# Kernel optimization log

Hardware: AMD Instinct MI355X
Metric: run time of the kernel (lower is better)

Reference implementation:

```python
import jax, jax.numpy as jnp
import numpy as np

EMBED_DIM = 512
NUM_HEADS = 8
HEAD_DIM = EMBED_DIM // NUM_HEADS  # 64


def setup_inputs() -> dict:
    key = jax.random.key(0)
    ks = jax.random.split(key, 11)
    B, S, E, dh = 4, 2048, EMBED_DIM, HEAD_DIM
    s_small = 1.0 / np.sqrt(dh)
    s_big = 1.0 / np.sqrt(E)
    return {
        "Q": jax.random.normal(ks[0], (B, S, E), jnp.float32),
        "K": jax.random.normal(ks[1], (B, S, E), jnp.float32),
        "V": jax.random.normal(ks[2], (B, S, E), jnp.float32),
        "Wq_w": jax.random.normal(ks[3], (dh, dh), jnp.float32) * s_small,
        "Wq_b": jnp.zeros((dh,), jnp.float32),
        "Wk_w": jax.random.normal(ks[4], (dh, dh), jnp.float32) * s_small,
        "Wk_b": jnp.zeros((dh,), jnp.float32),
        "Wv_w": jax.random.normal(ks[5], (dh, dh), jnp.float32) * s_small,
        "Wv_b": jnp.zeros((dh,), jnp.float32),
        "Wo_w": jax.random.normal(ks[6], (E, E), jnp.float32) * s_big,
        "Wo_b": jnp.zeros((E,), jnp.float32),
    }


def reference(Q, K, V, Wq_w, Wq_b, Wk_w, Wk_b, Wv_w, Wv_b, Wo_w, Wo_b):
    B, S, E = Q.shape
    H, dh = NUM_HEADS, HEAD_DIM
    # split heads: [B,S,E] -> [B,S,H,dh]; per-head shared linear (torch y = x @ W.T + b)
    q = jnp.einsum('bshd,od->bsho', Q.reshape(B, S, H, dh), Wq_w) + Wq_b
    k = jnp.einsum('bshd,od->bsho', K.reshape(B, S, H, dh), Wk_w) + Wk_b
    v = jnp.einsum('bshd,od->bsho', V.reshape(B, S, H, dh), Wv_w) + Wv_b
    # [B,H,S,dh]
    q = q.transpose(0, 2, 1, 3)
    k = k.transpose(0, 2, 1, 3)
    v = v.transpose(0, 2, 1, 3)
    scores = jnp.einsum('bhqd,bhkd->bhqk', q, k) / np.sqrt(dh)  # full N x N scores (faithful to naive impl)
    probs = jax.nn.softmax(scores, axis=-1)
    attn = jnp.einsum('bhqk,bhkd->bhqd', probs, v)
    # combine heads: [B,H,S,dh] -> [B,S,E]
    out = attn.transpose(0, 2, 1, 3).reshape(B, S, E)
    return out @ Wo_w.T + Wo_b
```

## Files before the change

kernel.cpp:

```cpp
#include <hip/hip_runtime.h>

typedef float  f32x4  __attribute__((ext_vector_type(4)));
typedef float  f32x16 __attribute__((ext_vector_type(16)));
typedef short  s16x8  __attribute__((ext_vector_type(8)));

constexpr int Bn = 4, Sn = 2048, En = 512, Hn = 8;
constexpr int BH = Bn * Hn;
constexpr int NT = Sn / 64;
constexpr float QSCL = 0.125f * 1.44269504088896f;

static __device__ __forceinline__ ushort f2bf(float f) {
  union { float f; uint u; } v; v.f = f;
  uint r = v.u + 0x7fffu + ((v.u >> 16) & 1u);
  return (ushort)(r >> 16);
}
static __device__ __forceinline__ uint2 pack4(float a, float b, float c, float d) {
  union { ushort us[4]; uint2 u; } pk;
  pk.us[0] = f2bf(a); pk.us[1] = f2bf(b); pk.us[2] = f2bf(c); pk.us[3] = f2bf(d);
  return pk.u;
}
static __device__ __forceinline__ float hexp2(float x) {
  float r; asm("v_exp_f32 %0, %1" : "=v"(r) : "v"(x)); return r;
}
static __device__ __forceinline__ uint pkbf(float lo, float hi2) {
  uint r; asm("v_cvt_pk_bf16_f32 %0, %1, %2" : "=v"(r) : "v"(lo), "v"(hi2)); return r;
}
#define SWAP32(a, b) asm("v_permlane32_swap_b32 %0, %1" : "+v"(a), "+v"(b))
static __device__ __forceinline__ s16x8 mk8(uint a, uint b, uint c, uint d) {
  union { uint u[4]; s16x8 v; } x; x.u[0] = a; x.u[1] = b; x.u[2] = c; x.u[3] = d; return x.v;
}
#define MFMA32(A, B, C) __builtin_amdgcn_mfma_f32_32x32x16_bf16((A), (B), (C), 0, 0, 0)
#define MFMA16(A, B, C) __builtin_amdgcn_mfma_f32_16x16x32_bf16((A), (B), (C), 0, 0, 0)
#define GLDS(SRC, DST) __builtin_amdgcn_global_load_lds( \
    (const __attribute__((address_space(1))) void*)(SRC), \
    (__attribute__((address_space(3))) void*)(DST), 16, 0, 0)

__global__ __launch_bounds__(256) void proj_kernel(
    const float* __restrict__ Qi, const float* __restrict__ Ki, const float* __restrict__ Vi,
    const float* __restrict__ Wq, const float* __restrict__ bq,
    const float* __restrict__ Wk, const float* __restrict__ bk,
    const float* __restrict__ Wv, const float* __restrict__ bv,
    ushort* __restrict__ qo, ushort* __restrict__ ko, ushort* __restrict__ vto)
{
  constexpr int LP = 72;
  __shared__ ushort Xl[64 * LP];
  __shared__ ushort Wl[64 * LP];
  const int role = blockIdx.z;
  const float* X    = role == 0 ? Qi : (role == 1 ? Ki : Vi);
  const float* W    = role == 0 ? Wq : (role == 1 ? Wk : Wv);
  const float* bias = role == 0 ? bq : (role == 1 ? bk : bv);
  const float oscl  = role == 0 ? QSCL : 1.0f;
  const int t = threadIdx.x, lane = t & 63, w = t >> 6;
  const int g = lane >> 4, ql = lane & 15;
  const int bh = blockIdx.y, b = bh >> 3, h = bh & 7;
  const int s0 = blockIdx.x * 64;

  {
    const int row = t >> 4, c = t & 15;
#pragma unroll
    for (int p = 0; p < 4; ++p) {
      const int rr = row + p * 16;
      const float4 wv = *(const float4*)(W + rr * 64 + c * 4);
      *(uint2*)&Wl[rr * LP + c * 4] = pack4(wv.x, wv.y, wv.z, wv.w);
      const float4 xv = *(const float4*)(X + ((size_t)b * Sn + s0 + rr) * En + h * 64 + c * 4);
      *(uint2*)&Xl[rr * LP + c * 4] = pack4(xv.x, xv.y, xv.z, xv.w);
    }
  }
  __syncthreads();

  f32x4 acc[4];
#pragma unroll
  for (int i = 0; i < 4; ++i) acc[i] = (f32x4){0.f, 0.f, 0.f, 0.f};
#pragma unroll
  for (int kc = 0; kc < 2; ++kc) {
    const s16x8 bfrag = *(const s16x8*)&Xl[(w * 16 + ql) * LP + kc * 32 + g * 8];
#pragma unroll
    for (int nt = 0; nt < 4; ++nt) {
      const s16x8 afrag = *(const s16x8*)&Wl[(nt * 16 + ql) * LP + kc * 32 + g * 8];
      acc[nt] = MFMA16(afrag, bfrag, acc[nt]);
    }
  }

  const int s = s0 + w * 16 + ql;
  if (role < 2) {
    ushort* dst = (role == 0 ? qo : ko) + ((size_t)bh * Sn + s) * 64;
#pragma unroll
    for (int nt = 0; nt < 4; ++nt) {
      const int ob = nt * 16 + g * 4;
      *(uint2*)&dst[ob] = pack4((acc[nt][0] + bias[ob]) * oscl, (acc[nt][1] + bias[ob + 1]) * oscl,
                                (acc[nt][2] + bias[ob + 2]) * oscl, (acc[nt][3] + bias[ob + 3]) * oscl);
    }
  } else {
#pragma unroll
    for (int nt = 0; nt < 4; ++nt) {
#pragma unroll
      for (int r = 0; r < 4; ++r) {
        const int o = nt * 16 + g * 4 + r;
        vto[((size_t)bh * 64 + o) * Sn + s] = f2bf(acc[nt][r] + bias[o]);
      }
    }
  }
}

__global__ __launch_bounds__(512, 4) void flash_kernel(
    const ushort* __restrict__ q, const ushort* __restrict__ k,
    const ushort* __restrict__ vt, ushort* __restrict__ attn)
{
  __shared__ __align__(16) char smem[36864];
  float* mrg = (float*)smem;
  const int tid = threadIdx.x, lane = tid & 63, w = tid >> 6;
  const int m = lane & 31, hi = lane >> 5;
  const int wl = w & 3, h2 = w >> 2;
  const int hx  = hi ^ (m & 7);
  const int hxv = hx ^ (h2 << 2);

  int lid = blockIdx.x + (blockIdx.y << 4);
  lid = (lid & 7) * 64 + (lid >> 3);
  const int bq = lid & 15, bh = lid >> 4;
  const int qrow = bq * 128 + wl * 32 + m;
  const int b = bh >> 3, h = bh & 7;

  const ushort* qp = q + ((size_t)bh * Sn + qrow) * 64 + hi * 8;
  const s16x8 qf0 = *(const s16x8*)(qp + 0);
  const s16x8 qf1 = *(const s16x8*)(qp + 16);
  const s16x8 qf2 = *(const s16x8*)(qp + 32);
  const s16x8 qf3 = *(const s16x8*)(qp + 48);

  const int srow = tid >> 3, sc = tid & 7, scs = sc ^ (srow & 7);
  const ushort* kS = k  + (size_t)bh * Sn * 64 + (size_t)srow * 64 + scs * 8;
  const ushort* vS = vt + ((size_t)bh * 64 + srow) * Sn + scs * 8;
  const uint dO = (uint)(tid * 16);
  char* KB0 = smem;          char* KB1 = smem + 8192;
  char* VB0 = smem + 16384;  char* VB1 = smem + 24576;

  const f32x16 z16 = {};
  f32x16 acc0 = {}, acc1 = {}, asum = {};
  union { ushort us[8]; s16x8 v; } onesU;
#pragma unroll
  for (int i = 0; i < 8; ++i) onesU.us[i] = 0x3F80;
  const s16x8 ones = onesU.v;

  GLDS(kS, KB0 + dO); GLDS(vS, VB0 + dO);
  kS += 4096; vS += 64;

#define LDK(KB, S)     (*(const s16x8*)((KB)  + ((h2 * 32 + m) * 64 + (((2 * (S)) ^ hx ) << 3)) * 2))
#define LDV(VB, DT, S) (*(const s16x8*)((VB)  + (((DT) * 32 + m) * 64 + (((2 * (S)) ^ hxv) << 3)) * 2))

#define STEP(T, KB, VB, KBn, VBn) do {                                      \
    if ((T) < NT - 1) {                                                     \
      GLDS(kS, (KBn) + dO); GLDS(vS, (VBn) + dO);                           \
      kS += 4096; vS += 64;                                                 \
      asm volatile("s_waitcnt vmcnt(2)" ::: "memory");                      \
    } else {                                                                \
      asm volatile("s_waitcnt vmcnt(0)" ::: "memory");                      \
    }                                                                       \
    __builtin_amdgcn_s_barrier();                                           \
    __builtin_amdgcn_sched_barrier(0);                                      \
    f32x16 sta, stb;                                                        \
    __builtin_amdgcn_s_setprio(1);                                          \
    sta = MFMA32(LDK(KB, 0), qf0, z16);                                     \
    sta = MFMA32(LDK(KB, 1), qf1, sta);                                     \
    stb = MFMA32(LDK(KB, 2), qf2, z16);                                     \
    stb = MFMA32(LDK(KB, 3), qf3, stb);                                     \
    __builtin_amdgcn_s_setprio(0);                                          \
    f32x16 p;                                                               \
    _Pragma("unroll")                                                       \
    for (int i = 0; i < 16; ++i) p[i] = hexp2(sta[i] + stb[i]);             \
    uint uA, uB, uC, uD, uE, uF, uG, uH;                                    \
    uA = pkbf(p[0], p[1]);   uB = pkbf(p[4], p[5]);   SWAP32(uA, uB);       \
    uC = pkbf(p[2], p[3]);   uD = pkbf(p[6], p[7]);   SWAP32(uC, uD);       \
    uE = pkbf(p[8], p[9]);   uF = pkbf(p[12], p[13]); SWAP32(uE, uF);       \
    uG = pkbf(p[10], p[11]); uH = pkbf(p[14], p[15]); SWAP32(uG, uH);       \
    const s16x8 pb0 = mk8(uA, uC, uB, uD);                                  \
    const s16x8 pb1 = mk8(uE, uG, uF, uH);                                  \
    __builtin_amdgcn_s_setprio(1);                                          \
    acc0 = MFMA32(LDV(VB, 0, 0), pb0, acc0);                                \
    acc0 = MFMA32(LDV(VB, 0, 1), pb1, acc0);                                \
    acc1 = MFMA32(LDV(VB, 1, 0), pb0, acc1);                                \
    acc1 = MFMA32(LDV(VB, 1, 1), pb1, acc1);                                \
    asum = MFMA32(ones, pb0, asum);                                         \
    asum = MFMA32(ones, pb1, asum);                                         \
    __builtin_amdgcn_s_setprio(0);                                          \
    __builtin_amdgcn_s_barrier();                                           \
    __builtin_amdgcn_sched_barrier(0);                                      \
  } while (0)

  for (int T = 0; T < NT; T += 2) {
    STEP(T,     KB0, VB0, KB1, VB1);
    STEP(T + 1, KB1, VB1, KB0, VB0);
  }
#undef STEP
#undef LDK
#undef LDV

  const float lT = asum[0];
  float* mp = mrg + (size_t)(wl * 64 + lane) * 36;
  __syncthreads();
  if (h2) {
#pragma unroll
    for (int i = 0; i < 4; ++i) {
      f32x4 t0 = {acc0[4 * i], acc0[4 * i + 1], acc0[4 * i + 2], acc0[4 * i + 3]};
      f32x4 t1 = {acc1[4 * i], acc1[4 * i + 1], acc1[4 * i + 2], acc1[4 * i + 3]};
      *(f32x4*)(mp + 4 * i) = t0;
      *(f32x4*)(mp + 16 + 4 * i) = t1;
    }
    mp[32] = lT;
  }
  __syncthreads();
  if (!h2) {
    const float inv = 1.0f / (lT + mp[32]);
    ushort* ap = attn + ((size_t)(b * Sn + qrow)) * En + h * 64;
#pragma unroll
    for (int g2 = 0; g2 < 4; ++g2) {
      float a0 = (acc0[g2 * 4 + 0] + mp[g2 * 4 + 0]) * inv;
      float a1 = (acc0[g2 * 4 + 1] + mp[g2 * 4 + 1]) * inv;
      float a2 = (acc0[g2 * 4 + 2] + mp[g2 * 4 + 2]) * inv;
      float a3 = (acc0[g2 * 4 + 3] + mp[g2 * 4 + 3]) * inv;
      float c0 = (acc1[g2 * 4 + 0] + mp[16 + g2 * 4 + 0]) * inv;
      float c1 = (acc1[g2 * 4 + 1] + mp[16 + g2 * 4 + 1]) * inv;
      float c2 = (acc1[g2 * 4 + 2] + mp[16 + g2 * 4 + 2]) * inv;
      float c3 = (acc1[g2 * 4 + 3] + mp[16 + g2 * 4 + 3]) * inv;
      uint2 u0, u1;
      u0.x = pkbf(a0, a1); u0.y = pkbf(a2, a3);
      u1.x = pkbf(c0, c1); u1.y = pkbf(c2, c3);
      *(uint2*)&ap[g2 * 8 + hi * 4]      = u0;
      *(uint2*)&ap[32 + g2 * 8 + hi * 4] = u1;
    }
  }
}

__global__ __launch_bounds__(512) void outproj_kernel(
    const ushort* __restrict__ attn, const float* __restrict__ Wo,
    const float* __restrict__ bo, float* __restrict__ out)
{
  constexpr int LP = 72;
  __shared__ ushort Al[128 * LP];
  __shared__ ushort Wl[128 * LP];
  const int t = threadIdx.x, lane = t & 63, w = t >> 6;
  const int g = lane >> 4, ml = lane & 15;
  const int wm = w >> 2, wn = w & 3;
  const int m0 = blockIdx.x * 128, n0 = blockIdx.y * 128;
  f32x4 acc[4][2];
#pragma unroll
  for (int i = 0; i < 4; ++i)
#pragma unroll
    for (int j = 0; j < 2; ++j) acc[i][j] = (f32x4){0.f, 0.f, 0.f, 0.f};

  const int srow = t >> 2, c0 = t & 3;
  for (int e0 = 0; e0 < En; e0 += 64) {
    __syncthreads();
#pragma unroll
    for (int p = 0; p < 2; ++p) {
      const int c = c0 + p * 4;
      const uint4 v = *(const uint4*)(attn + ((size_t)(m0 + srow)) * En + e0 + c * 8);
      *(uint4*)&Al[srow * LP + c * 8] = v;
    }
#pragma unroll
    for (int p = 0; p < 4; ++p) {
      const int c = c0 + p * 4;
      const float4 v = *(const float4*)(Wo + ((size_t)(n0 + srow)) * En + e0 + c * 4);
      *(uint2*)&Wl[srow * LP + c * 4] = pack4(v.x, v.y, v.z, v.w);
    }
    __syncthreads();
#pragma unroll
    for (int kc = 0; kc < 2; ++kc) {
      s16x8 bfr[4];
#pragma unroll
      for (int mf = 0; mf < 4; ++mf)
        bfr[mf] = *(const s16x8*)&Al[(wm * 64 + mf * 16 + ml) * LP + kc * 32 + g * 8];
#pragma unroll
      for (int nf = 0; nf < 2; ++nf) {
        const s16x8 afr = *(const s16x8*)&Wl[(wn * 32 + nf * 16 + ml) * LP + kc * 32 + g * 8];
#pragma unroll
        for (int mf = 0; mf < 4; ++mf)
          acc[mf][nf] = MFMA16(afr, bfr[mf], acc[mf][nf]);
      }
    }
  }
#pragma unroll
  for (int mf = 0; mf < 4; ++mf) {
    const int mrow = m0 + wm * 64 + mf * 16 + ml;
#pragma unroll
    for (int nf = 0; nf < 2; ++nf) {
      const int ncol = n0 + wn * 32 + nf * 16 + g * 4;
      const float4 bias = *(const float4*)(bo + ncol);
      float4 o;
      o.x = acc[mf][nf][0] + bias.x;
      o.y = acc[mf][nf][1] + bias.y;
      o.z = acc[mf][nf][2] + bias.z;
      o.w = acc[mf][nf][3] + bias.w;
      *(float4*)&out[(size_t)mrow * En + ncol] = o;
    }
  }
}

extern "C" void kernel_launch(void* const* d_in, const int* in_sizes, int n_in,
                              void* d_out, int out_size, void* d_ws, size_t ws_size,
                              hipStream_t stream) {
  const float* Qi = (const float*)d_in[0];
  const float* Ki = (const float*)d_in[1];
  const float* Vi = (const float*)d_in[2];
  const float* Wq = (const float*)d_in[3];
  const float* bq = (const float*)d_in[4];
  const float* Wk = (const float*)d_in[5];
  const float* bk = (const float*)d_in[6];
  const float* Wv = (const float*)d_in[7];
  const float* bv = (const float*)d_in[8];
  const float* Wo = (const float*)d_in[9];
  const float* bo = (const float*)d_in[10];

  const size_t TEN = (size_t)BH * Sn * 64;
  ushort* qw  = (ushort*)d_ws;
  ushort* kw  = qw + TEN;
  ushort* vtw = kw + TEN;
  ushort* at  = vtw + TEN;

  proj_kernel<<<dim3(Sn / 64, BH, 3), 256, 0, stream>>>(
      Qi, Ki, Vi, Wq, bq, Wk, bk, Wv, bv, qw, kw, vtw);
  flash_kernel<<<dim3(16, 32), 512, 0, stream>>>(qw, kw, vtw, at);
  outproj_kernel<<<dim3(Bn * Sn / 128, En / 128), 512, 0, stream>>>(
      at, Wo, bo, (float*)d_out);
}
```

Baseline: 84.96 us.

## Process two KV tiles per barrier stage with doubled shared-memory buffers

Restructures the flash attention KV loop so that each pipeline stage loads and processes 128 keys (two 64-key tiles) instead of 64. Shared memory grows from 36KB to 64KB to hold two double-buffered pairs of K and V tiles. This halves the number of barrier pairs and waitcnt points, which is meant to cut synchronization overhead and allow more in-flight loads. The larger LDS footprint may reduce how many blocks can be resident per CU compared with the launch-bounds target of 4.

```diff
diff --git a/kernel.cpp b/kernel.cpp
--- a/kernel.cpp
+++ b/kernel.cpp
@@ -6,7 +6,7 @@
 
 constexpr int Bn = 4, Sn = 2048, En = 512, Hn = 8;
 constexpr int BH = Bn * Hn;
-constexpr int NT = Sn / 64;
+constexpr int NT2 = Sn / 128;
 constexpr float QSCL = 0.125f * 1.44269504088896f;
 
 static __device__ __forceinline__ ushort f2bf(float f) {
@@ -106,7 +106,7 @@
     const ushort* __restrict__ q, const ushort* __restrict__ k,
     const ushort* __restrict__ vt, ushort* __restrict__ attn)
 {
-  __shared__ __align__(16) char smem[36864];
+  __shared__ __align__(16) char smem[65536];
   float* mrg = (float*)smem;
   const int tid = threadIdx.x, lane = tid & 63, w = tid >> 6;
   const int m = lane & 31, hi = lane >> 5;
@@ -130,8 +130,10 @@
   const ushort* kS = k  + (size_t)bh * Sn * 64 + (size_t)srow * 64 + scs * 8;
   const ushort* vS = vt + ((size_t)bh * 64 + srow) * Sn + scs * 8;
   const uint dO = (uint)(tid * 16);
-  char* KB0 = smem;          char* KB1 = smem + 8192;
-  char* VB0 = smem + 16384;  char* VB1 = smem + 24576;
+  char* K0a = smem;          char* K0b = smem + 8192;
+  char* V0a = smem + 16384;  char* V0b = smem + 24576;
+  char* K1a = smem + 32768;  char* K1b = smem + 40960;
+  char* V1a = smem + 49152;  char* V1b = smem + 57344;
 
   const f32x16 z16 = {};
   f32x16 acc0 = {}, acc1 = {}, asum = {};
@@ -140,22 +142,18 @@
   for (int i = 0; i < 8; ++i) onesU.us[i] = 0x3F80;
   const s16x8 ones = onesU.v;
 
-  GLDS(kS, KB0 + dO); GLDS(vS, VB0 + dO);
-  kS += 4096; vS += 64;
-
-#define LDK(KB, S)     (*(const s16x8*)((KB)  + ((h2 * 32 + m) * 64 + (((2 * (S)) ^ hx ) << 3)) * 2))
-#define LDV(VB, DT, S) (*(const s16x8*)((VB)  + (((DT) * 32 + m) * 64 + (((2 * (S)) ^ hxv) << 3)) * 2))
-
-#define STEP(T, KB, VB, KBn, VBn) do {                                      \
-    if ((T) < NT - 1) {                                                     \
-      GLDS(kS, (KBn) + dO); GLDS(vS, (VBn) + dO);                           \
-      kS += 4096; vS += 64;                                                 \
-      asm volatile("s_waitcnt vmcnt(2)" ::: "memory");                      \
-    } else {                                                                \
-      asm volatile("s_waitcnt vmcnt(0)" ::: "memory");                      \
-    }                                                                       \
-    __builtin_amdgcn_s_barrier();                                           \
-    __builtin_amdgcn_sched_barrier(0);                                      \
+#define STAGE(KA, KBB, VA, VBB) do {                                        \
+    GLDS(kS, (KA) + dO);  GLDS(kS + 4096, (KBB) + dO);                      \
+    GLDS(vS, (VA) + dO);  GLDS(vS + 64,   (VBB) + dO);                      \
+    kS += 8192; vS += 128;                                                  \
+  } while (0)
+
+  STAGE(K0a, K0b, V0a, V0b);
+
+#define LDK(KB, S)     (*(const s16x8*)((KB) + ((h2 * 32 + m) * 64 + (((2 * (S)) ^ hx ) << 3)) * 2))
+#define LDV(VB, DT, S) (*(const s16x8*)((VB) + (((DT) * 32 + m) * 64 + (((2 * (S)) ^ hxv) << 3)) * 2))
+
+#define HALF(KB, VB) do {                                                   \
     f32x16 sta, stb;                                                        \
     __builtin_amdgcn_s_setprio(1);                                          \
     sta = MFMA32(LDK(KB, 0), qf0, z16);                                     \
@@ -181,17 +179,32 @@
     asum = MFMA32(ones, pb0, asum);                                         \
     asum = MFMA32(ones, pb1, asum);                                         \
     __builtin_amdgcn_s_setprio(0);                                          \
+  } while (0)
+
+#define STEP(T, KA, KBB, VA, VBB, NKA, NKB, NVA, NVB) do {                  \
+    if ((T) < NT2 - 1) {                                                    \
+      STAGE(NKA, NKB, NVA, NVB);                                            \
+      asm volatile("s_waitcnt vmcnt(4)" ::: "memory");                      \
+    } else {                                                                \
+      asm volatile("s_waitcnt vmcnt(0)" ::: "memory");                      \
+    }                                                                       \
+    __builtin_amdgcn_s_barrier();                                           \
+    __builtin_amdgcn_sched_barrier(0);                                      \
+    HALF(KA, VA);                                                           \
+    HALF(KBB, VBB);                                                         \
     __builtin_amdgcn_s_barrier();                                           \
     __builtin_amdgcn_sched_barrier(0);                                      \
   } while (0)
 
-  for (int T = 0; T < NT; T += 2) {
-    STEP(T,     KB0, VB0, KB1, VB1);
-    STEP(T + 1, KB1, VB1, KB0, VB0);
+  for (int T = 0; T < NT2; T += 2) {
+    STEP(T,     K0a, K0b, V0a, V0b, K1a, K1b, V1a, V1b);
+    STEP(T + 1, K1a, K1b, V1a, V1b, K0a, K0b, V0a, V0b);
   }
 #undef STEP
+#undef HALF
 #undef LDK
 #undef LDV
+#undef STAGE
 
   const float lT = asum[0];
   float* mp = mrg + (size_t)(wl * 64 + lane) * 36;
```

Measured after the change: 132.7 us. 56.2% more time.
